# Kernel optimization log

Measured on AMD Instinct MI355X. Metric: run time of the kernel, lower is better.

Reference implementation:

```python
import jax, jax.numpy as jnp
import numpy as np

N, E = 50000, 400000
DIN, DH, H, DOUT = 128, 32, 10, 32
HID = H * DH
NEG = 0.2          # LeakyReLU slope in GATv2
EPS_BN = 1e-5

def setup_inputs():
    key = jax.random.key(0)
    ks = jax.random.split(key, 10)
    g = lambda k, shape, fan: jax.random.normal(k, shape, jnp.float32) * (1.0 / np.sqrt(fan))
    return {
        "x": jax.random.normal(ks[0], (N, DIN), jnp.float32),
        "edge_index": jax.random.randint(ks[1], (2, E), 0, N),
        "Wl1": g(ks[2], (DIN, HID), DIN), "bl1": jnp.zeros((HID,), jnp.float32),
        "Wr1": g(ks[3], (DIN, HID), DIN), "br1": jnp.zeros((HID,), jnp.float32),
        "att1": g(ks[4], (H, DH), DH),   "bias1": jnp.zeros((HID,), jnp.float32),
        "gamma": jnp.ones((HID,), jnp.float32), "beta": jnp.zeros((HID,), jnp.float32),
        "prelu_a": jnp.asarray(0.25, jnp.float32),
        "Wl2": g(ks[5], (HID, DOUT), HID), "bl2": jnp.zeros((DOUT,), jnp.float32),
        "Wr2": g(ks[6], (HID, DOUT), HID), "br2": jnp.zeros((DOUT,), jnp.float32),
        "att2": g(ks[7], (1, DOUT), DOUT), "bias2": jnp.zeros((DOUT,), jnp.float32),
    }

def gatv2_layer(x, src, dst, Wl, bl, Wr, br, att, bias, heads, ch, concat):
    n = x.shape[0]
    xl = (x @ Wl + bl).reshape(n, heads, ch)   # source-side (message) transform
    xr = (x @ Wr + br).reshape(n, heads, ch)   # target-side transform
    e = jax.nn.leaky_relu(xl[src] + xr[dst], NEG)          # [E,H,C]
    score = jnp.einsum('ehc,hc->eh', e, att)               # [E,H]
    m = jax.ops.segment_max(score, dst, num_segments=n)    # segment softmax (stable)
    a = jnp.exp(score - m[dst])
    denom = jax.ops.segment_sum(a, dst, num_segments=n)
    alpha = a / (denom[dst] + 1e-16)                       # [E,H]
    out = jax.ops.segment_sum(xl[src] * alpha[:, :, None], dst, num_segments=n)  # [N,H,C]
    out = out.reshape(n, heads * ch) if concat else out.mean(axis=1)
    return out + bias

def reference(x, edge_index, Wl1, bl1, Wr1, br1, att1, bias1, gamma, beta, prelu_a, Wl2, bl2, Wr2, br2, att2, bias2):
    src, dst = edge_index[0], edge_index[1]
    h = gatv2_layer(x, src, dst, Wl1, bl1, Wr1, br1, att1, bias1, H, DH, True)
    mu = h.mean(axis=0)
    var = h.var(axis=0)                                    # BatchNorm1d, batch stats
    h = (h - mu) * jax.lax.rsqrt(var + EPS_BN) * gamma + beta
    h = jnp.where(h >= 0, h, prelu_a * h)                  # PReLU (single shared a)
    out = gatv2_layer(h, src, dst, Wl2, bl2, Wr2, br2, att2, bias2, 1, DOUT, False)
    return out, jax.nn.log_softmax(out, axis=1)
```

## Files before the change

kernel.cpp:

```cpp
#include <hip/hip_runtime.h>
#include <hip/hip_bf16.h>

#define NN 50000
#define NE 400000
#define DIN 128
#define DH 32
#define NH 10
#define HID 320
#define DOUT 32
#define NEG_SLOPE 0.2f
#define EPS_BN 1e-5f

typedef __attribute__((ext_vector_type(8))) short short8;
typedef __attribute__((ext_vector_type(4))) float f32x4;

__device__ inline unsigned short f2bf(float f) {
    unsigned int u = __float_as_uint(f);
    u += 0x7fffu + ((u >> 16) & 1u);
    return (unsigned short)(u >> 16);
}
__device__ inline float bf2f(unsigned short u) {
    return __uint_as_float(((unsigned int)u) << 16);
}
__device__ inline float bflo(unsigned int u) { return __uint_as_float(u << 16); }
__device__ inline float bfhi(unsigned int u) { return __uint_as_float(u & 0xffff0000u); }
__device__ inline float lrelu(float x) { return fmaxf(x, NEG_SLOPE * x); }

__global__ __launch_bounds__(256) void precast_x(const float* __restrict__ x,
        unsigned short* __restrict__ xb) {
    int i = blockIdx.x * 256 + threadIdx.x;
    if (i < NN * DIN / 4) {
        float4 v = *(const float4*)(x + (size_t)i * 4);
        ushort4 s;
        s.x = f2bf(v.x); s.y = f2bf(v.y); s.z = f2bf(v.z); s.w = f2bf(v.w);
        *(ushort4*)(xb + (size_t)i * 4) = s;
    }
}

__global__ void precast_w1(const float* __restrict__ Wl, const float* __restrict__ Wr,
        unsigned short* __restrict__ wlt, unsigned short* __restrict__ wrt) {
    int idx = blockIdx.x * 256 + threadIdx.x;
    if (idx < HID * DIN) {
        int c = idx >> 7, k = idx & 127;
        wlt[idx] = f2bf(Wl[(size_t)k * HID + c]);
        wrt[idx] = f2bf(Wr[(size_t)k * HID + c]);
    }
}

__global__ void precast_w2(const float* __restrict__ Wl2, const float* __restrict__ Wr2,
        unsigned short* __restrict__ wl2t, unsigned short* __restrict__ wr2t) {
    int idx = blockIdx.x * 256 + threadIdx.x;
    if (idx < HID * DOUT) {
        int c = idx / HID, k = idx - c * HID;
        wl2t[idx] = f2bf(Wl2[k * DOUT + c]);
        wr2t[idx] = f2bf(Wr2[k * DOUT + c]);
    }
}

__global__ __launch_bounds__(256) void gemm1_kernel(
    const unsigned short* __restrict__ xb,
    const unsigned short* __restrict__ wlt, const unsigned short* __restrict__ wrt,
    const float* __restrict__ bl, const float* __restrict__ br,
    unsigned short* __restrict__ xl1, unsigned short* __restrict__ xr1)
{
    __shared__ short xs[64 * 128];
    int b = blockIdx.x;
    int xcd = b & 7, j = b >> 3;
    int base = (xcd < 4) ? xcd * 978 : 3912 + (xcd - 4) * 977;
    int t = base + j;
    int r0 = (t / 10) * 64;
    int c0 = (t % 10) * 32;

    const int tid = threadIdx.x;
    for (int i = tid; i < 2048; i += 256) {
        int rr = i >> 5;
        int u4 = (i & 31) << 2;
        ushort4 v = make_ushort4(0, 0, 0, 0);
        if (r0 + rr < NN) v = *(const ushort4*)(xb + (size_t)(r0 + rr) * DIN + u4);
        int u = (rr * 128 + u4) ^ ((rr & 7) << 3);
        *(ushort4*)&xs[u] = v;
    }
    __syncthreads();

    const int w = tid >> 6, lane = tid & 63;
    const int row16 = lane & 15;
    const int kgrp = (lane >> 4) << 3;
    const int arow = w * 16 + row16;
    const unsigned short* bLp = wlt + (size_t)(c0 + row16) * DIN + kgrp;
    const unsigned short* bRp = wrt + (size_t)(c0 + row16) * DIN + kgrp;

    f32x4 acc00 = {}, acc01 = {}, acc10 = {}, acc11 = {};
    #pragma unroll
    for (int kk = 0; kk < 4; ++kk) {
        int au = (arow * 128 + kk * 32 + kgrp) ^ ((arow & 7) << 3);
        short8 a = *(short8*)&xs[au];
        short8 bL0 = *(const short8*)(bLp + kk * 32);
        short8 bL1 = *(const short8*)(bLp + 16 * DIN + kk * 32);
        short8 bR0 = *(const short8*)(bRp + kk * 32);
        short8 bR1 = *(const short8*)(bRp + 16 * DIN + kk * 32);
        acc00 = __builtin_amdgcn_mfma_f32_16x16x32_bf16(a, bL0, acc00, 0, 0, 0);
        acc01 = __builtin_amdgcn_mfma_f32_16x16x32_bf16(a, bL1, acc01, 0, 0, 0);
        acc10 = __builtin_amdgcn_mfma_f32_16x16x32_bf16(a, bR0, acc10, 0, 0, 0);
        acc11 = __builtin_amdgcn_mfma_f32_16x16x32_bf16(a, bR1, acc11, 0, 0, 0);
    }
    const int orow = r0 + w * 16 + ((lane >> 4) << 2);
    #pragma unroll
    for (int cf = 0; cf < 2; ++cf) {
        const int col = c0 + cf * 16 + row16;
        const float blv = bl[col], brv = br[col];
        const f32x4 aL = cf ? acc01 : acc00;
        const f32x4 aR = cf ? acc11 : acc10;
        #pragma unroll
        for (int reg = 0; reg < 4; ++reg) {
            int row = orow + reg;
            if (row < NN) {
                xl1[(size_t)row * HID + col] = f2bf(aL[reg] + blv);
                xr1[(size_t)row * HID + col] = f2bf(aR[reg] + brv);
            }
        }
    }
}

__global__ void hist_kernel(const int* __restrict__ dst, int* __restrict__ deg) {
    int e = blockIdx.x * blockDim.x + threadIdx.x;
    if (e < NE) atomicAdd(&deg[dst[e]], 1);
}

__global__ __launch_bounds__(1024) void scan1_kernel(const int* __restrict__ deg,
        int* __restrict__ tmp, int* __restrict__ bsum) {
    __shared__ int s[1024];
    const int tid = threadIdx.x;
    int i = blockIdx.x * 1024 + tid;
    int v = (i < NN) ? deg[i] : 0;
    s[tid] = v;
    __syncthreads();
    for (int off = 1; off < 1024; off <<= 1) {
        int u = (tid >= off) ? s[tid - off] : 0;
        __syncthreads();
        s[tid] += u;
        __syncthreads();
    }
    if (i < NN) tmp[i] = s[tid];
    if (tid == 1023) bsum[blockIdx.x] = s[1023];
}

__global__ void scan2_kernel(const int* __restrict__ bsum, int* __restrict__ boff) {
    int lane = threadIdx.x;
    int v = (lane < 49) ? bsum[lane] : 0;
    for (int off = 1; off < 64; off <<= 1) {
        int u = __shfl_up(v, off);
        if (lane >= off) v += u;
    }
    int excl = __shfl_up(v, 1);
    if (lane == 0) excl = 0;
    if (lane < 49) boff[lane] = excl;
}

__global__ __launch_bounds__(1024) void scan3_kernel(const int* __restrict__ deg,
        const int* __restrict__ tmp, const int* __restrict__ boff,
        int* __restrict__ row_ptr, int* __restrict__ cursor) {
    int i = blockIdx.x * 1024 + threadIdx.x;
    if (i < NN) {
        int incl = tmp[i] + boff[blockIdx.x];
        int st = incl - deg[i];
        row_ptr[i] = st;
        cursor[i] = st;
        if (i == NN - 1) row_ptr[NN] = incl;
    }
}

__global__ void scatter_kernel(const int* __restrict__ src, const int* __restrict__ dst,
        int* __restrict__ cursor, int* __restrict__ sorted_src) {
    int e = blockIdx.x * blockDim.x + threadIdx.x;
    if (e < NE) {
        int d = dst[e];
        int p = atomicAdd(&cursor[d], 1);
        sorted_src[p] = src[e];
    }
}

__global__ __launch_bounds__(320) void agg1_kernel(
    const unsigned short* __restrict__ xl1, const unsigned short* __restrict__ xr1,
    const int* __restrict__ row_ptr, const int* __restrict__ sorted_src,
    const float* __restrict__ att1, const float* __restrict__ bias1,
    unsigned short* __restrict__ h1b)
{
    const int t = threadIdx.x;
    const int nsub = t / 80;
    const int r = t - nsub * 80;
    const int h = r >> 3;
    const int l8 = r & 7;
    const int c0 = h * 32 + l8 * 4;
    const int n = blockIdx.x * 4 + nsub;

    const float4 at = *(const float4*)(att1 + c0);
    const unsigned rbase = (unsigned)n * HID + c0;
    uint2 xr4 = *(const uint2*)(xr1 + rbase);
    const float xr0 = bflo(xr4.x), xr1f = bfhi(xr4.x);
    const float xr2 = bflo(xr4.y), xr3 = bfhi(xr4.y);

    const int rp = row_ptr[n];
    const int deg = row_ptr[n + 1] - rp;
    const int* sp = sorted_src + rp;

    float l = 0.f, ac0 = 0.f, ac1 = 0.f, ac2 = 0.f, ac3 = 0.f;
    int i = 0;
    for (; i + 2 <= deg; i += 2) {
        unsigned offA = (unsigned)sp[i] * HID + c0;
        unsigned offB = (unsigned)sp[i + 1] * HID + c0;
        uint2 ua = *(const uint2*)(xl1 + offA);
        uint2 ub = *(const uint2*)(xl1 + offB);
        float xA0 = bflo(ua.x), xA1 = bfhi(ua.x), xA2 = bflo(ua.y), xA3 = bfhi(ua.y);
        float xB0 = bflo(ub.x), xB1 = bfhi(ub.x), xB2 = bflo(ub.y), xB3 = bfhi(ub.y);
        float vA = lrelu(xA0 + xr0) * at.x;
        vA = fmaf(lrelu(xA1 + xr1f), at.y, vA);
        vA = fmaf(lrelu(xA2 + xr2), at.z, vA);
        vA = fmaf(lrelu(xA3 + xr3), at.w, vA);
        float vB = lrelu(xB0 + xr0) * at.x;
        vB = fmaf(lrelu(xB1 + xr1f), at.y, vB);
        vB = fmaf(lrelu(xB2 + xr2), at.z, vB);
        vB = fmaf(lrelu(xB3 + xr3), at.w, vB);
        vA += __shfl_xor(vA, 1); vB += __shfl_xor(vB, 1);
        vA += __shfl_xor(vA, 2); vB += __shfl_xor(vB, 2);
        vA += __shfl_xor(vA, 4); vB += __shfl_xor(vB, 4);
        float pA = __expf(vA), pB = __expf(vB);
        l += pA + pB;
        ac0 = fmaf(pA, xA0, ac0); ac0 = fmaf(pB, xB0, ac0);
        ac1 = fmaf(pA, xA1, ac1); ac1 = fmaf(pB, xB1, ac1);
        ac2 = fmaf(pA, xA2, ac2); ac2 = fmaf(pB, xB2, ac2);
        ac3 = fmaf(pA, xA3, ac3); ac3 = fmaf(pB, xB3, ac3);
    }
    if (i < deg) {
        unsigned offA = (unsigned)sp[i] * HID + c0;
        uint2 ua = *(const uint2*)(xl1 + offA);
        float xA0 = bflo(ua.x), xA1 = bfhi(ua.x), xA2 = bflo(ua.y), xA3 = bfhi(ua.y);
        float vA = lrelu(xA0 + xr0) * at.x;
        vA = fmaf(lrelu(xA1 + xr1f), at.y, vA);
        vA = fmaf(lrelu(xA2 + xr2), at.z, vA);
        vA = fmaf(lrelu(xA3 + xr3), at.w, vA);
        vA += __shfl_xor(vA, 1);
        vA += __shfl_xor(vA, 2);
        vA += __shfl_xor(vA, 4);
        float pA = __expf(vA);
        l += pA;
        ac0 = fmaf(pA, xA0, ac0); ac1 = fmaf(pA, xA1, ac1);
        ac2 = fmaf(pA, xA2, ac2); ac3 = fmaf(pA, xA3, ac3);
    }
    const float inv = 1.f / (l + 1e-16f);
    const float4 bi = *(const float4*)(bias1 + c0);
    uint2 outp;
    outp.x = (unsigned)f2bf(ac0 * inv + bi.x) | ((unsigned)f2bf(ac1 * inv + bi.y) << 16);
    outp.y = (unsigned)f2bf(ac2 * inv + bi.z) | ((unsigned)f2bf(ac3 * inv + bi.w) << 16);
    *(uint2*)(h1b + rbase) = outp;
}

__global__ __launch_bounds__(320) void bnpart_kernel(const unsigned short* __restrict__ h1b,
        float* __restrict__ ps, float* __restrict__ pq) {
    const int c = threadIdx.x;
    float s = 0.f, q = 0.f;
    for (int n = blockIdx.x; n < NN; n += gridDim.x) {
        float v = bf2f(h1b[(size_t)n * HID + c]);
        s += v;
        q = fmaf(v, v, q);
    }
    ps[(size_t)blockIdx.x * HID + c] = s;
    pq[(size_t)blockIdx.x * HID + c] = q;
}

__global__ void bnfinal_kernel(const float* __restrict__ ps, const float* __restrict__ pq,
        const float* __restrict__ gamma, const float* __restrict__ beta,
        float* __restrict__ scale, float* __restrict__ shift) {
    int c = threadIdx.x;
    double S = 0.0, Q = 0.0;
    for (int b = 0; b < 1024; ++b) {
        S += (double)ps[(size_t)b * HID + c];
        Q += (double)pq[(size_t)b * HID + c];
    }
    double mean = S / (double)NN;
    double var  = Q / (double)NN - mean * mean;
    float sc = gamma[c] * rsqrtf((float)var + EPS_BN);
    scale[c] = sc;
    shift[c] = beta[c] - (float)mean * sc;
}

__global__ __launch_bounds__(256) void gemm2_kernel(
    const unsigned short* __restrict__ h1b,
    const float* __restrict__ scale, const float* __restrict__ shift,
    const float* __restrict__ prelu_a,
    const unsigned short* __restrict__ wl2t, const unsigned short* __restrict__ wr2t,
    const float* __restrict__ bl2, const float* __restrict__ br2,
    float* __restrict__ xl2, float* __restrict__ xr2)
{
    __shared__ short hs[64 * 320];
    const int tid = threadIdx.x;
    const int r0 = blockIdx.x * 64;
    const float a = prelu_a[0];
    for (int f = tid; f < 5120; f += 256) {
        int e = f << 2;
        int rr = e / 320;
        int cc = e - rr * 320;
        ushort4 hv = make_ushort4(0, 0, 0, 0);
        if (r0 + rr < NN) hv = *(const ushort4*)(h1b + (size_t)(r0 + rr) * HID + cc);
        float4 sc = *(const float4*)(scale + cc);
        float4 sh = *(const float4*)(shift + cc);
        float o0 = bf2f(hv.x) * sc.x + sh.x; o0 = (o0 >= 0.f) ? o0 : a * o0;
        float o1 = bf2f(hv.y) * sc.y + sh.y; o1 = (o1 >= 0.f) ? o1 : a * o1;
        float o2 = bf2f(hv.z) * sc.z + sh.z; o2 = (o2 >= 0.f) ? o2 : a * o2;
        float o3 = bf2f(hv.w) * sc.w + sh.w; o3 = (o3 >= 0.f) ? o3 : a * o3;
        short4 s;
        s.x = (short)f2bf(o0); s.y = (short)f2bf(o1);
        s.z = (short)f2bf(o2); s.w = (short)f2bf(o3);
        int u = (rr * 320 + cc) ^ ((rr & 7) << 3);
        *(short4*)&hs[u] = s;
    }
    __syncthreads();

    const int w = tid >> 6, lane = tid & 63;
    const int arow = w * 16 + (lane & 15);
    const int kgrp = (lane >> 4) << 3;
    const int bcol = lane & 15;
    f32x4 acc00 = {}, acc01 = {}, acc10 = {}, acc11 = {};
    #pragma unroll
    for (int kk = 0; kk < 10; ++kk) {
        int au = (arow * 320 + kk * 32 + kgrp) ^ ((arow & 7) << 3);
        short8 afr = *(short8*)&hs[au];
        const int ko = kk * 32 + kgrp;
        short8 bL0 = *(const short8*)(wl2t + bcol * HID + ko);
        short8 bL1 = *(const short8*)(wl2t + (16 + bcol) * HID + ko);
        short8 bR0 = *(const short8*)(wr2t + bcol * HID + ko);
        short8 bR1 = *(const short8*)(wr2t + (16 + bcol) * HID + ko);
        acc00 = __builtin_amdgcn_mfma_f32_16x16x32_bf16(afr, bL0, acc00, 0, 0, 0);
        acc01 = __builtin_amdgcn_mfma_f32_16x16x32_bf16(afr, bL1, acc01, 0, 0, 0);
        acc10 = __builtin_amdgcn_mfma_f32_16x16x32_bf16(afr, bR0, acc10, 0, 0, 0);
        acc11 = __builtin_amdgcn_mfma_f32_16x16x32_bf16(afr, bR1, acc11, 0, 0, 0);
    }
    const int orow = r0 + w * 16 + ((lane >> 4) << 2);
    #pragma unroll
    for (int cf = 0; cf < 2; ++cf) {
        const int col = cf * 16 + bcol;
        const float blv = bl2[col], brv = br2[col];
        const f32x4 aL = cf ? acc01 : acc00;
        const f32x4 aR = cf ? acc11 : acc10;
        #pragma unroll
        for (int reg = 0; reg < 4; ++reg) {
            int row = orow + reg;
            if (row < NN) {
                xl2[(size_t)row * DOUT + col] = aL[reg] + blv;
                xr2[(size_t)row * DOUT + col] = aR[reg] + brv;
            }
        }
    }
}

__global__ __launch_bounds__(256) void agg2_kernel(
    const float* __restrict__ xl2, const float* __restrict__ xr2,
    const int* __restrict__ row_ptr, const int* __restrict__ sorted_src,
    const float* __restrict__ att2, const float* __restrict__ bias2,
    float* __restrict__ out)
{
    const int t = threadIdx.x;
    const int nsub = t >> 3;
    const int l8 = t & 7;
    const int c0 = l8 * 4;
    const int n = blockIdx.x * 32 + nsub;
    if (n >= NN) return;

    const float4 at = *(const float4*)(att2 + c0);
    const float4 xr4 = *(const float4*)(xr2 + (size_t)n * DOUT + c0);
    const int rp = row_ptr[n];
    const int deg = row_ptr[n + 1] - rp;
    const int* sp = sorted_src + rp;

    float l = 0.f, ac0 = 0.f, ac1 = 0.f, ac2 = 0.f, ac3 = 0.f;
    int i = 0;
    for (; i + 2 <= deg; i += 2) {
        unsigned offA = (unsigned)sp[i] * DOUT + c0;
        unsigned offB = (unsigned)sp[i + 1] * DOUT + c0;
        float4 xa = *(const float4*)(xl2 + offA);
        float4 xb = *(const float4*)(xl2 + offB);
        float vA = lrelu(xa.x + xr4.x) * at.x;
        vA = fmaf(lrelu(xa.y + xr4.y), at.y, vA);
        vA = fmaf(lrelu(xa.z + xr4.z), at.z, vA);
        vA = fmaf(lrelu(xa.w + xr4.w), at.w, vA);
        float vB = lrelu(xb.x + xr4.x) * at.x;
        vB = fmaf(lrelu(xb.y + xr4.y), at.y, vB);
        vB = fmaf(lrelu(xb.z + xr4.z), at.z, vB);
        vB = fmaf(lrelu(xb.w + xr4.w), at.w, vB);
        vA += __shfl_xor(vA, 1); vB += __shfl_xor(vB, 1);
        vA += __shfl_xor(vA, 2); vB += __shfl_xor(vB, 2);
        vA += __shfl_xor(vA, 4); vB += __shfl_xor(vB, 4);
        float pA = __expf(vA), pB = __expf(vB);
        l += pA + pB;
        ac0 = fmaf(pA, xa.x, ac0); ac0 = fmaf(pB, xb.x, ac0);
        ac1 = fmaf(pA, xa.y, ac1); ac1 = fmaf(pB, xb.y, ac1);
        ac2 = fmaf(pA, xa.z, ac2); ac2 = fmaf(pB, xb.z, ac2);
        ac3 = fmaf(pA, xa.w, ac3); ac3 = fmaf(pB, xb.w, ac3);
    }
    if (i < deg) {
        unsigned offA = (unsigned)sp[i] * DOUT + c0;
        float4 xa = *(const float4*)(xl2 + offA);
        float vA = lrelu(xa.x + xr4.x) * at.x;
        vA = fmaf(lrelu(xa.y + xr4.y), at.y, vA);
        vA = fmaf(lrelu(xa.z + xr4.z), at.z, vA);
        vA = fmaf(lrelu(xa.w + xr4.w), at.w, vA);
        vA += __shfl_xor(vA, 1);
        vA += __shfl_xor(vA, 2);
        vA += __shfl_xor(vA, 4);
        float pA = __expf(vA);
        l += pA;
        ac0 = fmaf(pA, xa.x, ac0); ac1 = fmaf(pA, xa.y, ac1);
        ac2 = fmaf(pA, xa.z, ac2); ac3 = fmaf(pA, xa.w, ac3);
    }
    const float inv = 1.f / (l + 1e-16f);
    const float4 bi = *(const float4*)(bias2 + c0);
    float o0 = ac0 * inv + bi.x;
    float o1 = ac1 * inv + bi.y;
    float o2 = ac2 * inv + bi.z;
    float o3 = ac3 * inv + bi.w;
    float mx = fmaxf(fmaxf(o0, o1), fmaxf(o2, o3));
    mx = fmaxf(mx, __shfl_xor(mx, 1));
    mx = fmaxf(mx, __shfl_xor(mx, 2));
    mx = fmaxf(mx, __shfl_xor(mx, 4));
    float se = __expf(o0 - mx) + __expf(o1 - mx) + __expf(o2 - mx) + __expf(o3 - mx);
    se += __shfl_xor(se, 1);
    se += __shfl_xor(se, 2);
    se += __shfl_xor(se, 4);
    float lse = mx + __logf(se);
    float4 ov; ov.x = o0; ov.y = o1; ov.z = o2; ov.w = o3;
    *(float4*)(out + (size_t)n * DOUT + c0) = ov;
    float4 lv; lv.x = o0 - lse; lv.y = o1 - lse; lv.z = o2 - lse; lv.w = o3 - lse;
    *(float4*)(out + (size_t)(NN + n) * DOUT + c0) = lv;
}

extern "C" void kernel_launch(void* const* d_in, const int* in_sizes, int n_in,
                              void* d_out, int out_size, void* d_ws, size_t ws_size,
                              hipStream_t stream)
{
    const float* x       = (const float*)d_in[0];
    const int*   ei      = (const int*)d_in[1];
    const float* Wl1     = (const float*)d_in[2];
    const float* bl1     = (const float*)d_in[3];
    const float* Wr1     = (const float*)d_in[4];
    const float* br1     = (const float*)d_in[5];
    const float* att1    = (const float*)d_in[6];
    const float* bias1   = (const float*)d_in[7];
    const float* gamma   = (const float*)d_in[8];
    const float* beta    = (const float*)d_in[9];
    const float* prelu_a = (const float*)d_in[10];
    const float* Wl2     = (const float*)d_in[11];
    const float* bl2     = (const float*)d_in[12];
    const float* Wr2     = (const float*)d_in[13];
    const float* br2     = (const float*)d_in[14];
    const float* att2    = (const float*)d_in[15];
    const float* bias2   = (const float*)d_in[16];
    const int* src = ei;
    const int* dst = ei + NE;

    char* w = (char*)d_ws;
    unsigned short* xl1b = (unsigned short*)w;
    unsigned short* xr1b = xl1b + (size_t)NN * HID;
    unsigned short* h1b  = xr1b + (size_t)NN * HID;
    char* sm = w + 96000000ull;
    float* scale   = (float*)(sm + 5120);
    float* shift   = (float*)(sm + 6400);
    unsigned short* wl2t = (unsigned short*)(sm + 7680);
    unsigned short* wr2t = (unsigned short*)(sm + 28160);
    unsigned short* wlt1 = (unsigned short*)(sm + 48640);
    unsigned short* wrt1 = (unsigned short*)(sm + 130560);
    int* deg     = (int*)(sm + 212480);
    int* cursor  = (int*)(sm + 412480);
    int* sorted  = (int*)(sm + 612480);
    int* row_ptr = (int*)(sm + 2212480);
    int* tmp     = (int*)(sm + 2412484);
    int* bsum    = (int*)(sm + 2612484);
    int* boff    = (int*)(sm + 2612740);
    unsigned short* xb = (unsigned short*)(sm + 3000000);
    float* bn_ps = (float*)(sm + 16000000);
    float* bn_pq = (float*)(sm + 18000000);
    float* xl2 = (float*)w;
    float* xr2 = (float*)(w + (size_t)NN * DOUT * 4);

    hipMemsetAsync(deg, 0, NN * sizeof(int), stream);

    precast_x<<<(NN * DIN / 4 + 255) / 256, 256, 0, stream>>>(x, xb);
    precast_w1<<<(HID * DIN + 255) / 256, 256, 0, stream>>>(Wl1, Wr1, wlt1, wrt1);
    precast_w2<<<(HID * DOUT + 255) / 256, 256, 0, stream>>>(Wl2, Wr2, wl2t, wr2t);
    hist_kernel<<<(NE + 255) / 256, 256, 0, stream>>>(dst, deg);
    gemm1_kernel<<<7820, 256, 0, stream>>>(xb, wlt1, wrt1, bl1, br1, xl1b, xr1b);
    scan1_kernel<<<49, 1024, 0, stream>>>(deg, tmp, bsum);
    scan2_kernel<<<1, 64, 0, stream>>>(bsum, boff);
    scan3_kernel<<<49, 1024, 0, stream>>>(deg, tmp, boff, row_ptr, cursor);
    scatter_kernel<<<(NE + 255) / 256, 256, 0, stream>>>(src, dst, cursor, sorted);
    agg1_kernel<<<NN / 4, 320, 0, stream>>>(xl1b, xr1b, row_ptr, sorted, att1, bias1, h1b);
    bnpart_kernel<<<1024, HID, 0, stream>>>(h1b, bn_ps, bn_pq);
    bnfinal_kernel<<<1, HID, 0, stream>>>(bn_ps, bn_pq, gamma, beta, scale, shift);
    gemm2_kernel<<<(NN + 63) / 64, 256, 0, stream>>>(h1b, scale, shift, prelu_a,
        wl2t, wr2t, bl2, br2, xl2, xr2);
    agg2_kernel<<<(NN + 31) / 32, 256, 0, stream>>>(xl2, xr2, row_ptr, sorted, att2, bias2,
        (float*)d_out);
}
```

Before: 424.8 us.

## Fuse x bf16 cast into gemm1 and compute all column tiles per block

Removes the separate precast_x kernel and its bf16 intermediate buffer. The fp32-to-bf16 conversion now happens while gemm1 loads its x tile into LDS. Each block now computes all 10 column tiles for its 64 rows, so x is read only once instead of ten times, and the A fragments are kept in registers. The MFMA operands are swapped so each lane holds 4 contiguous output columns, which allows vectorized ushort4 stores and float4 bias loads. In exchange the grid shrinks to 782 blocks with longer serial work per block, which reduces parallelism and latency hiding on a large GPU.

```diff
diff --git a/kernel.cpp b/kernel.cpp
--- a/kernel.cpp
+++ b/kernel.cpp
@@ -26,17 +26,6 @@
 __device__ inline float bfhi(unsigned int u) { return __uint_as_float(u & 0xffff0000u); }
 __device__ inline float lrelu(float x) { return fmaxf(x, NEG_SLOPE * x); }
 
-__global__ __launch_bounds__(256) void precast_x(const float* __restrict__ x,
-        unsigned short* __restrict__ xb) {
-    int i = blockIdx.x * 256 + threadIdx.x;
-    if (i < NN * DIN / 4) {
-        float4 v = *(const float4*)(x + (size_t)i * 4);
-        ushort4 s;
-        s.x = f2bf(v.x); s.y = f2bf(v.y); s.z = f2bf(v.z); s.w = f2bf(v.w);
-        *(ushort4*)(xb + (size_t)i * 4) = s;
-    }
-}
-
 __global__ void precast_w1(const float* __restrict__ Wl, const float* __restrict__ Wr,
         unsigned short* __restrict__ wlt, unsigned short* __restrict__ wrt) {
     int idx = blockIdx.x * 256 + threadIdx.x;
@@ -58,65 +47,79 @@
 }
 
 __global__ __launch_bounds__(256) void gemm1_kernel(
-    const unsigned short* __restrict__ xb,
+    const float* __restrict__ x,
     const unsigned short* __restrict__ wlt, const unsigned short* __restrict__ wrt,
     const float* __restrict__ bl, const float* __restrict__ br,
     unsigned short* __restrict__ xl1, unsigned short* __restrict__ xr1)
 {
     __shared__ short xs[64 * 128];
-    int b = blockIdx.x;
-    int xcd = b & 7, j = b >> 3;
-    int base = (xcd < 4) ? xcd * 978 : 3912 + (xcd - 4) * 977;
-    int t = base + j;
-    int r0 = (t / 10) * 64;
-    int c0 = (t % 10) * 32;
-
     const int tid = threadIdx.x;
+    const int r0 = blockIdx.x * 64;
+
     for (int i = tid; i < 2048; i += 256) {
-        int rr = i >> 5;
-        int u4 = (i & 31) << 2;
-        ushort4 v = make_ushort4(0, 0, 0, 0);
-        if (r0 + rr < NN) v = *(const ushort4*)(xb + (size_t)(r0 + rr) * DIN + u4);
-        int u = (rr * 128 + u4) ^ ((rr & 7) << 3);
-        *(ushort4*)&xs[u] = v;
+        int rr = i >> 5, c4 = (i & 31) << 2;
+        float4 v = make_float4(0.f, 0.f, 0.f, 0.f);
+        if (r0 + rr < NN) v = *(const float4*)(x + (size_t)(r0 + rr) * DIN + c4);
+        short4 s;
+        s.x = (short)f2bf(v.x); s.y = (short)f2bf(v.y);
+        s.z = (short)f2bf(v.z); s.w = (short)f2bf(v.w);
+        int u = (rr * 128 + c4) ^ ((rr & 7) << 3);
+        *(short4*)&xs[u] = s;
     }
     __syncthreads();
 
     const int w = tid >> 6, lane = tid & 63;
-    const int row16 = lane & 15;
+    const int l16 = lane & 15;
     const int kgrp = (lane >> 4) << 3;
-    const int arow = w * 16 + row16;
-    const unsigned short* bLp = wlt + (size_t)(c0 + row16) * DIN + kgrp;
-    const unsigned short* bRp = wrt + (size_t)(c0 + row16) * DIN + kgrp;
-
-    f32x4 acc00 = {}, acc01 = {}, acc10 = {}, acc11 = {};
+    const int xrow_l = w * 16 + l16;
+    const int grow = r0 + xrow_l;
+
+    short8 afr[4];
     #pragma unroll
     for (int kk = 0; kk < 4; ++kk) {
-        int au = (arow * 128 + kk * 32 + kgrp) ^ ((arow & 7) << 3);
-        short8 a = *(short8*)&xs[au];
-        short8 bL0 = *(const short8*)(bLp + kk * 32);
-        short8 bL1 = *(const short8*)(bLp + 16 * DIN + kk * 32);
-        short8 bR0 = *(const short8*)(bRp + kk * 32);
-        short8 bR1 = *(const short8*)(bRp + 16 * DIN + kk * 32);
-        acc00 = __builtin_amdgcn_mfma_f32_16x16x32_bf16(a, bL0, acc00, 0, 0, 0);
-        acc01 = __builtin_amdgcn_mfma_f32_16x16x32_bf16(a, bL1, acc01, 0, 0, 0);
-        acc10 = __builtin_amdgcn_mfma_f32_16x16x32_bf16(a, bR0, acc10, 0, 0, 0);
-        acc11 = __builtin_amdgcn_mfma_f32_16x16x32_bf16(a, bR1, acc11, 0, 0, 0);
-    }
-    const int orow = r0 + w * 16 + ((lane >> 4) << 2);
+        int au = (xrow_l * 128 + kk * 32 + kgrp) ^ ((xrow_l & 7) << 3);
+        afr[kk] = *(short8*)&xs[au];
+    }
+
+    const bool rok = grow < NN;
+    const int mcol = (lane >> 4) << 2;
     #pragma unroll
-    for (int cf = 0; cf < 2; ++cf) {
-        const int col = c0 + cf * 16 + row16;
-        const float blv = bl[col], brv = br[col];
-        const f32x4 aL = cf ? acc01 : acc00;
-        const f32x4 aR = cf ? acc11 : acc10;
+    for (int ct = 0; ct < 10; ++ct) {
+        const int c0 = ct * 32;
+        const unsigned short* wl0 = wlt + (size_t)(c0 + l16) * DIN + kgrp;
+        const unsigned short* wr0 = wrt + (size_t)(c0 + l16) * DIN + kgrp;
+        f32x4 aL0 = {}, aL1 = {}, aR0 = {}, aR1 = {};
         #pragma unroll
-        for (int reg = 0; reg < 4; ++reg) {
-            int row = orow + reg;
-            if (row < NN) {
-                xl1[(size_t)row * HID + col] = f2bf(aL[reg] + blv);
-                xr1[(size_t)row * HID + col] = f2bf(aR[reg] + brv);
-            }
+        for (int kk = 0; kk < 4; ++kk) {
+            short8 bL0 = *(const short8*)(wl0 + kk * 32);
+            short8 bL1 = *(const short8*)(wl0 + 16 * DIN + kk * 32);
+            short8 bR0 = *(const short8*)(wr0 + kk * 32);
+            short8 bR1 = *(const short8*)(wr0 + 16 * DIN + kk * 32);
+            aL0 = __builtin_amdgcn_mfma_f32_16x16x32_bf16(bL0, afr[kk], aL0, 0, 0, 0);
+            aL1 = __builtin_amdgcn_mfma_f32_16x16x32_bf16(bL1, afr[kk], aL1, 0, 0, 0);
+            aR0 = __builtin_amdgcn_mfma_f32_16x16x32_bf16(bR0, afr[kk], aR0, 0, 0, 0);
+            aR1 = __builtin_amdgcn_mfma_f32_16x16x32_bf16(bR1, afr[kk], aR1, 0, 0, 0);
+        }
+        if (rok) {
+            const int cb0 = c0 + mcol;
+            const int cb1 = cb0 + 16;
+            float4 b0 = *(const float4*)(bl + cb0);
+            float4 b1 = *(const float4*)(bl + cb1);
+            ushort4 s0, s1;
+            s0.x = f2bf(aL0[0] + b0.x); s0.y = f2bf(aL0[1] + b0.y);
+            s0.z = f2bf(aL0[2] + b0.z); s0.w = f2bf(aL0[3] + b0.w);
+            s1.x = f2bf(aL1[0] + b1.x); s1.y = f2bf(aL1[1] + b1.y);
+            s1.z = f2bf(aL1[2] + b1.z); s1.w = f2bf(aL1[3] + b1.w);
+            *(ushort4*)(xl1 + (size_t)grow * HID + cb0) = s0;
+            *(ushort4*)(xl1 + (size_t)grow * HID + cb1) = s1;
+            b0 = *(const float4*)(br + cb0);
+            b1 = *(const float4*)(br + cb1);
+            s0.x = f2bf(aR0[0] + b0.x); s0.y = f2bf(aR0[1] + b0.y);
+            s0.z = f2bf(aR0[2] + b0.z); s0.w = f2bf(aR0[3] + b0.w);
+            s1.x = f2bf(aR1[0] + b1.x); s1.y = f2bf(aR1[1] + b1.y);
+            s1.z = f2bf(aR1[2] + b1.z); s1.w = f2bf(aR1[3] + b1.w);
+            *(ushort4*)(xr1 + (size_t)grow * HID + cb0) = s0;
+            *(ushort4*)(xr1 + (size_t)grow * HID + cb1) = s1;
         }
     }
 }
@@ -474,7 +477,6 @@
     int* tmp     = (int*)(sm + 2412484);
     int* bsum    = (int*)(sm + 2612484);
     int* boff    = (int*)(sm + 2612740);
-    unsigned short* xb = (unsigned short*)(sm + 3000000);
     float* bn_ps = (float*)(sm + 16000000);
     float* bn_pq = (float*)(sm + 18000000);
     float* xl2 = (float*)w;
@@ -482,11 +484,10 @@
 
     hipMemsetAsync(deg, 0, NN * sizeof(int), stream);
 
-    precast_x<<<(NN * DIN / 4 + 255) / 256, 256, 0, stream>>>(x, xb);
     precast_w1<<<(HID * DIN + 255) / 256, 256, 0, stream>>>(Wl1, Wr1, wlt1, wrt1);
     precast_w2<<<(HID * DOUT + 255) / 256, 256, 0, stream>>>(Wl2, Wr2, wl2t, wr2t);
     hist_kernel<<<(NE + 255) / 256, 256, 0, stream>>>(dst, deg);
-    gemm1_kernel<<<7820, 256, 0, stream>>>(xb, wlt1, wrt1, bl1, br1, xl1b, xr1b);
+    gemm1_kernel<<<782, 256, 0, stream>>>(x, wlt1, wrt1, bl1, br1, xl1b, xr1b);
     scan1_kernel<<<49, 1024, 0, stream>>>(deg, tmp, bsum);
     scan2_kernel<<<1, 64, 0, stream>>>(bsum, boff);
     scan3_kernel<<<49, 1024, 0, stream>>>(deg, tmp, boff, row_ptr, cursor);
```

Measured after the change: 426.9 us. No clear change (+0.5%).
